# Kernel optimization log

Measured on AMD Instinct MI355X. Metric: run time of the kernel, lower is better.

## Reference

```python
import jax, jax.numpy as jnp
import numpy as np

DIM = 1024
NUM_HEADS = 16
HEAD_DIM = DIM // NUM_HEADS


def setup_inputs() -> dict:
    key = jax.random.key(0)
    k_x, k_q, k_k, k_v, k_o = jax.random.split(key, 5)
    B, L = 2, 2048
    scale = 1.0 / np.sqrt(DIM)
    x_bld = jax.random.normal(k_x, (B, L, DIM), dtype=jnp.float32)
    # LinearGeneral kernels: (in_features, num_heads, head_dim) for q/k/v,
    # (num_heads, head_dim, out_features) for out. Init ~ lecun_normal-ish scale.
    Wq = jax.random.normal(k_q, (DIM, NUM_HEADS, HEAD_DIM), dtype=jnp.float32) * scale
    Wk = jax.random.normal(k_k, (DIM, NUM_HEADS, HEAD_DIM), dtype=jnp.float32) * scale
    Wv = jax.random.normal(k_v, (DIM, NUM_HEADS, HEAD_DIM), dtype=jnp.float32) * scale
    Wo = jax.random.normal(k_o, (NUM_HEADS, HEAD_DIM, DIM), dtype=jnp.float32) * scale
    return {"x_bld": x_bld, "Wq": Wq, "Wk": Wk, "Wv": Wv, "Wo": Wo}


def reference(x_bld, Wq, Wk, Wv, Wo) -> jnp.ndarray:
    # Projections: [B,L,D] x [D,H,hd] -> [B,L,H,hd]
    q_blhd = jnp.einsum('bld,dhk->blhk', x_bld, Wq)
    k_blhd = jnp.einsum('bld,dhk->blhk', x_bld, Wk)
    v_blhd = jnp.einsum('bld,dhk->blhk', x_bld, Wv)
    # Scores: [B,H,L,L]
    attn_bhll = jnp.einsum('bqhd,bkhd->bhqk', q_blhd, k_blhd)
    attn_bhll = attn_bhll / jnp.sqrt(jnp.asarray(HEAD_DIM, dtype=attn_bhll.dtype))
    L = x_bld.shape[1]
    qi = jnp.arange(L)[:, None]
    ki = jnp.arange(L)[None, :]
    mask_ll = ki <= qi  # causal, no window
    neg_inf = jnp.finfo(attn_bhll.dtype).min
    attn_bhll = jnp.where(mask_ll[None, None, :, :], attn_bhll, neg_inf)
    attn_bhll = jax.nn.softmax(attn_bhll, axis=-1)
    y_blhd = jnp.einsum('bhqk,bkhd->bqhd', attn_bhll, v_blhd)
    # Output projection: contract (H, hd) -> D
    return jnp.einsum('blhk,hkd->bld', y_blhd, Wo)
```

## Files before the change

### kernel.cpp

```cpp
#include <hip/hip_runtime.h>
#include <hip/hip_bf16.h>

typedef __hip_bfloat16 bf16;
typedef __attribute__((ext_vector_type(8))) short short8;
typedef __attribute__((ext_vector_type(4))) float f32x4;
typedef __attribute__((ext_vector_type(4))) unsigned int u32x4;

__device__ __forceinline__ float bfbits2f(unsigned short u) {
    return __uint_as_float(((unsigned int)u) << 16);
}
__device__ __forceinline__ unsigned short f2bfbits(float f) {
    union { float f; unsigned int u; } x;
    x.f = f;
    unsigned int r = x.u + 0x7FFFu + ((x.u >> 16) & 1u);
    return (unsigned short)(r >> 16);
}
__device__ __forceinline__ unsigned int pack_bf16x2(float lo, float hi) {
    unsigned int u0 = __float_as_uint(lo) + 0x8000u;
    unsigned int u1 = __float_as_uint(hi) + 0x8000u;
    return __builtin_amdgcn_perm(u1, u0, 0x07060302u);
}
__device__ __forceinline__ void async_copy16(const void* g, void* l) {
    __builtin_amdgcn_global_load_lds(
        (const __attribute__((address_space(1))) void*)g,
        (__attribute__((address_space(3))) void*)l, 16, 0, 0);
}
__device__ __forceinline__ bool sniff_bf16(const unsigned int* p, int lane) {
    unsigned int wd = p[lane];
    unsigned int e = (wd >> 7) & 0xFFu;
    return __popcll(__ballot(e >= 90u && e <= 150u)) > 40;
}

__global__ __launch_bounds__(256) void prep(
    const void* __restrict__ X, const void* __restrict__ W1,
    const void* __restrict__ W2, const void* __restrict__ W3,
    const void* __restrict__ W4, short* __restrict__ xb,
    short* __restrict__ O1, short* __restrict__ O2,
    short* __restrict__ O3, short* __restrict__ O4) {
    __shared__ float tbuf[32][33];
    const int bx = blockIdx.x;
    const int tid = threadIdx.x;
    const int lane = tid & 63;

    if (bx < 2048) {
        const bool isBf = sniff_bf16((const unsigned int*)X, lane);
        const int i = (bx * 256 + tid) * 8;
        if (isBf) {
            *(short8*)&xb[i] = *(const short8*)((const short*)X + i);
        } else {
            const float* xf = (const float*)X + i;
            float4 a = *(const float4*)xf;
            float4 b = *(const float4*)(xf + 4);
            short8 o;
            o[0] = (short)f2bfbits(a.x); o[1] = (short)f2bfbits(a.y);
            o[2] = (short)f2bfbits(a.z); o[3] = (short)f2bfbits(a.w);
            o[4] = (short)f2bfbits(b.x); o[5] = (short)f2bfbits(b.y);
            o[6] = (short)f2bfbits(b.z); o[7] = (short)f2bfbits(b.w);
            *(short8*)&xb[i] = o;
        }
    } else {
        const void* Ws[4] = {W1, W2, W3, W4};
        short* Os[4] = {O1, O2, O3, O4};
        const int t = bx - 2048;
        const int wsel = t >> 10;
        const int tile = t & 1023;
        const int bxt = tile & 31, byt = tile >> 5;
        const void* W = Ws[wsel];
        const bool isBf = sniff_bf16((const unsigned int*)W, lane);
        const float scale = (wsel == 0) ? 0.18033688f : 1.0f;
        short* O = Os[wsel];

        const int tx = tid & 31, ty = tid >> 5;
        const int gx = bxt * 32 + tx;
#pragma unroll
        for (int i = 0; i < 4; i++) {
            const int gy = byt * 32 + ty + i * 8;
            float v = isBf
                ? bfbits2f(((const unsigned short*)W)[(size_t)gy * 1024 + gx])
                : ((const float*)W)[(size_t)gy * 1024 + gx];
            tbuf[ty + i * 8][tx] = v * scale;
        }
        __syncthreads();
#pragma unroll
        for (int i = 0; i < 4; i++) {
            const int orow = bxt * 32 + ty + i * 8;
            const int ocol = byt * 32 + tx;
            O[(size_t)orow * 1024 + ocol] = (short)f2bfbits(tbuf[tx][ty + i * 8]);
        }
    }
}

__global__ __launch_bounds__(256) void transpose_v(const short* __restrict__ qkv,
                                                   short* __restrict__ VtG) {
    __shared__ short t[32][33];
    const int tx = threadIdx.x & 31, ty = threadIdx.x >> 5;
    const int b = blockIdx.z >> 4, h = blockIdx.z & 15;
    const int l0 = blockIdx.x * 32, d0 = blockIdx.y * 32;
#pragma unroll
    for (int i = 0; i < 4; i++) {
        const int l = l0 + ty + i * 8;
        t[ty + i * 8][tx] =
            qkv[(size_t)(b * 2048 + l) * 3072 + 2048 + h * 64 + d0 + tx];
    }
    __syncthreads();
    const int ptx = 2 * (tx & 15) + (tx >> 4);
#pragma unroll
    for (int i = 0; i < 4; i++) {
        const int d = d0 + ty + i * 8;
        VtG[((size_t)(b * 16 + h) * 64 + d) * 2048 + l0 + ptx] = t[tx][ty + i * 8];
    }
}

template <int BN>
__global__ __launch_bounds__(256) void gemm_async(const short* __restrict__ A,
                                                  const short* __restrict__ Bt,
                                                  void* __restrict__ C,
                                                  const unsigned int* __restrict__ xdet,
                                                  int M, int N, int K) {
    __shared__ short As[2][128 * 32];
    __shared__ short Bs[2][BN * 32];
    constexpr int NI = BN / 32;

    const int tid = threadIdx.x;
    const int lane = tid & 63;
    const int wv = __builtin_amdgcn_readfirstlane(tid >> 6);
    const int quad = lane >> 4, l16 = lane & 15;
    const int wr = wv >> 1, wc = wv & 1;
    const int m0 = blockIdx.y * 128, n0 = blockIdx.x * BN;

    const int gr = lane >> 2;
    const int gc = ((lane & 3) ^ ((lane >> 3) & 3)) * 8;

    const f32x4 zero = {0.f, 0.f, 0.f, 0.f};
    f32x4 acc[4][NI];
#pragma unroll
    for (int mi = 0; mi < 4; mi++)
#pragma unroll
        for (int ni = 0; ni < NI; ni++) acc[mi][ni] = zero;

    const short* aptr[2];
    const short* bptr[BN / 64];
#pragma unroll
    for (int t = 0; t < 2; t++)
        aptr[t] = A + (size_t)(m0 + t * 64 + wv * 16 + gr) * K + gc;
#pragma unroll
    for (int t = 0; t < BN / 64; t++)
        bptr[t] = Bt + (size_t)(n0 + t * 64 + wv * 16 + gr) * K + gc;

#pragma unroll
    for (int t = 0; t < 2; t++) async_copy16(aptr[t], &As[0][(t * 64 + wv * 16) * 32]);
#pragma unroll
    for (int t = 0; t < BN / 64; t++) async_copy16(bptr[t], &Bs[0][(t * 64 + wv * 16) * 32]);

    const int ss = (quad ^ ((l16 >> 1) & 3)) * 8;

    for (int k0 = 0; k0 < K; k0 += 32) {
        const int cur = (k0 >> 5) & 1;
        __syncthreads();
        if (k0 + 32 < K) {
            const int nxt = cur ^ 1;
#pragma unroll
            for (int t = 0; t < 2; t++)
                async_copy16(aptr[t] + k0 + 32, &As[nxt][(t * 64 + wv * 16) * 32]);
#pragma unroll
            for (int t = 0; t < BN / 64; t++)
                async_copy16(bptr[t] + k0 + 32, &Bs[nxt][(t * 64 + wv * 16) * 32]);
        }

        short8 af[4], bfv[NI];
#pragma unroll
        for (int mi = 0; mi < 4; mi++)
            af[mi] = *(const short8*)&As[cur][(wr * 64 + mi * 16 + l16) * 32 + ss];
#pragma unroll
        for (int ni = 0; ni < NI; ni++)
            bfv[ni] = *(const short8*)&Bs[cur][(wc * (BN / 2) + ni * 16 + l16) * 32 + ss];
#pragma unroll
        for (int mi = 0; mi < 4; mi++)
#pragma unroll
            for (int ni = 0; ni < NI; ni++)
                acc[mi][ni] = __builtin_amdgcn_mfma_f32_16x16x32_bf16(
                    af[mi], bfv[ni], acc[mi][ni], 0, 0, 0);
    }

    bool outBf = true;
    if (xdet) outBf = sniff_bf16(xdet, lane);
    if (outBf) {
        unsigned short* Cb = (unsigned short*)C;
#pragma unroll
        for (int mi = 0; mi < 4; mi++)
#pragma unroll
            for (int ni = 0; ni < NI; ni++)
#pragma unroll
                for (int r = 0; r < 4; r++) {
                    const int row = m0 + wr * 64 + mi * 16 + quad * 4 + r;
                    const int col = n0 + wc * (BN / 2) + ni * 16 + l16;
                    Cb[(size_t)row * N + col] = f2bfbits(acc[mi][ni][r]);
                }
    } else {
        float* Cf = (float*)C;
#pragma unroll
        for (int mi = 0; mi < 4; mi++)
#pragma unroll
            for (int ni = 0; ni < NI; ni++)
#pragma unroll
                for (int r = 0; r < 4; r++) {
                    const int row = m0 + wr * 64 + mi * 16 + quad * 4 + r;
                    const int col = n0 + wc * (BN / 2) + ni * 16 + l16;
                    Cf[(size_t)row * N + col] = acc[mi][ni][r];
                }
    }
}

__global__ __launch_bounds__(128) void attn_mfma8(
    const short* __restrict__ qkv, const short* __restrict__ VtG,
    short* __restrict__ Yg, short* __restrict__ Opart, float* __restrict__ ml) {
    __shared__ float scr[4][16][68];
    __shared__ float lred[2][64];

    const int tid = threadIdx.x;
    const int lane = tid & 63;
    const int wv = __builtin_amdgcn_readfirstlane(tid >> 6);
    const int quad = lane >> 4, l16 = lane & 15;
    const int bh = blockIdx.x;
    const int b = bh >> 4, h = bh & 15;

    int qb, seg, S;
    const int slot = blockIdx.y;
    if (slot < 64)      { qb = 31 - (slot >> 2); seg = slot & 3; S = 4; }
    else if (slot < 80) { const int t2 = slot - 64; qb = 15 - (t2 >> 1); seg = t2 & 1; S = 2; }
    else                { qb = 87 - slot; seg = 0; S = 1; }

    const int ns = qb + 1;
    const int sb0 = seg * ns / S;
    const int sb1 = (seg + 1) * ns / S;
    const int w32 = wv * 32;

    short8 qf[4][2];
    {
        const short* qbase = qkv + (size_t)(b * 2048 + qb * 64 + l16) * 3072 +
                             h * 64 + quad * 8;
#pragma unroll
        for (int qt = 0; qt < 4; qt++)
#pragma unroll
            for (int hf = 0; hf < 2; hf++)
                qf[qt][hf] = *(const short8*)(qbase + qt * 16 * 3072 + hf * 32);
    }

    const size_t KSTEP = (size_t)64 * 3072;
    const short* kb[2];
#pragma unroll
    for (int kt = 0; kt < 2; kt++)
        kb[kt] = qkv + (size_t)(b * 2048 + sb0 * 64 + w32 + kt * 16 + l16) * 3072 +
                 1024 + h * 64 + quad * 8;
    const short* vb[4];
#pragma unroll
    for (int dt = 0; dt < 4; dt++)
        vb[dt] = VtG + ((size_t)bh * 64 + dt * 16 + l16) * 2048 + sb0 * 64 + w32 +
                 quad * 8;

    f32x4 O[4][4];
#pragma unroll
    for (int qt = 0; qt < 4; qt++)
#pragma unroll
        for (int dt = 0; dt < 4; dt++) O[qt][dt] = {0.f, 0.f, 0.f, 0.f};
    float lp[4] = {0.f, 0.f, 0.f, 0.f};

    const f32x4 minit = {-17.3123405f, -17.3123405f, -17.3123405f, -17.3123405f};
    const int keyoff0 = w32 + quad * 4;

    auto LOADK = [&](short8 (&kf)[2][2], short8 (&vf)[4]) {
#pragma unroll
        for (int kt = 0; kt < 2; kt++) {
#pragma unroll
            for (int hf = 0; hf < 2; hf++)
                kf[kt][hf] = *(const short8*)(kb[kt] + hf * 32);
            kb[kt] += KSTEP;
        }
#pragma unroll
        for (int dt = 0; dt < 4; dt++) {
            vf[dt] = *(const short8*)vb[dt];
            vb[dt] += 64;
        }
    };

    auto COMPUTE = [&](const short8 (&kf)[2][2], const short8 (&vf)[4], int sb) {
#pragma unroll
        for (int qt = 0; qt < 4; qt++) {
            f32x4 sA = __builtin_amdgcn_mfma_f32_16x16x32_bf16(kf[0][0], qf[qt][0], minit, 0, 0, 0);
            sA = __builtin_amdgcn_mfma_f32_16x16x32_bf16(kf[0][1], qf[qt][1], sA, 0, 0, 0);
            f32x4 sB = __builtin_amdgcn_mfma_f32_16x16x32_bf16(kf[1][0], qf[qt][0], minit, 0, 0, 0);
            sB = __builtin_amdgcn_mfma_f32_16x16x32_bf16(kf[1][1], qf[qt][1], sB, 0, 0, 0);
            if (sb == qb) {
                const int qcol = qt * 16 + l16;
#pragma unroll
                for (int r = 0; r < 4; r++) {
                    if (keyoff0 + r > qcol) sA[r] = -1e30f;
                    if (keyoff0 + 16 + r > qcol) sB[r] = -1e30f;
                }
            }
            union { u32x4 u; short8 s; } pa;
#pragma unroll
            for (int t = 0; t < 4; t++) {
                sA[t] = __builtin_amdgcn_exp2f(sA[t]);
                sB[t] = __builtin_amdgcn_exp2f(sB[t]);
                lp[qt] += sA[t] + sB[t];
                pa.u[t] = pack_bf16x2(sA[t], sB[t]);
            }
#pragma unroll
            for (int dt = 0; dt < 4; dt++)
                O[qt][dt] = __builtin_amdgcn_mfma_f32_16x16x32_bf16(
                    pa.s, vf[dt], O[qt][dt], 0, 0, 0);
        }
    };

    short8 kA[2][2], vA[4], kB[2][2], vB[4];
    LOADK(kA, vA);
    int sb = sb0;
    while (true) {
        if (sb + 1 < sb1) LOADK(kB, vB);
        COMPUTE(kA, vA, sb);
        if (++sb >= sb1) break;
        if (sb + 1 < sb1) LOADK(kA, vA);
        COMPUTE(kB, vB, sb);
        if (++sb >= sb1) break;
    }

#pragma unroll
    for (int qt = 0; qt < 4; qt++) {
        float v = lp[qt];
        v += __shfl_xor(v, 16);
        v += __shfl_xor(v, 32);
        if (quad == 0) lred[wv][qt * 16 + l16] = v;
    }

#pragma unroll
    for (int qt = 0; qt < 4; qt++) {
        if ((qt >> 1) != wv) {
#pragma unroll
            for (int dt = 0; dt < 4; dt++)
#pragma unroll
                for (int r = 0; r < 4; r++)
                    scr[qt][quad * 4 + r][dt * 16 + l16] = O[qt][dt][r];
        }
    }
    __syncthreads();
#pragma unroll
    for (int qt = 0; qt < 4; qt++) {
        if ((qt >> 1) == wv) {
#pragma unroll
            for (int dt = 0; dt < 4; dt++)
#pragma unroll
                for (int r = 0; r < 4; r++)
                    O[qt][dt][r] += scr[qt][quad * 4 + r][dt * 16 + l16];
        }
    }

    if (S == 1) {
#pragma unroll
        for (int qt = 0; qt < 4; qt++) {
            if ((qt >> 1) == wv) {
#pragma unroll
                for (int r = 0; r < 4; r++) {
                    const int q = qt * 16 + quad * 4 + r;
                    const float inv = 1.f / (lred[0][q] + lred[1][q]);
#pragma unroll
                    for (int dt = 0; dt < 4; dt++)
                        Yg[(size_t)(b * 2048 + qb * 64 + q) * 1024 + h * 64 +
                           dt * 16 + l16] = (short)f2bfbits(O[qt][dt][r] * inv);
                }
            }
        }
    } else {
        const int qidx = qb - 8;
        const int base = ((seg * 32 + bh) * 24 + qidx) * 64;
#pragma unroll
        for (int qt = 0; qt < 4; qt++) {
            if ((qt >> 1) == wv) {
#pragma unroll
                for (int r = 0; r < 4; r++) {
                    const int q = qt * 16 + quad * 4 + r;
#pragma unroll
                    for (int dt = 0; dt < 4; dt++)
                        Opart[(size_t)(base + q) * 64 + dt * 16 + l16] =
                            (short)f2bfbits(O[qt][dt][r]);
                    if (l16 == 0) ml[base + q] = lred[0][q] + lred[1][q];
                }
            }
        }
    }
}

__global__ __launch_bounds__(256) void attn_combine6(
    const short* __restrict__ Opart, const float* __restrict__ ml,
    short* __restrict__ Yg) {
    const int qb = 8 + blockIdx.x;
    const int bh = blockIdx.y;
    const int b = bh >> 4, h = bh & 15;
    const int S = (qb >= 16) ? 4 : 2;
    const int qidx = qb - 8;
    const int tid = threadIdx.x;
    const int q = tid >> 2;
    const int d0 = (tid & 3) * 16;

    float a0[8] = {}, a1[8] = {};
    float lsum = 0.f;
    for (int s = 0; s < S; s++) {
        const int idx = ((s * 32 + bh) * 24 + qidx) * 64 + q;
        lsum += ml[idx];
        const short* p = Opart + (size_t)idx * 64 + d0;
        short8 x0 = *(const short8*)p;
        short8 x1 = *(const short8*)(p + 8);
#pragma unroll
        for (int t = 0; t < 8; t++) {
            a0[t] += bfbits2f((unsigned short)x0[t]);
            a1[t] += bfbits2f((unsigned short)x1[t]);
        }
    }
    const float inv = 1.f / lsum;
    short8 o0, o1;
#pragma unroll
    for (int t = 0; t < 8; t++) {
        o0[t] = (short)f2bfbits(a0[t] * inv);
        o1[t] = (short)f2bfbits(a1[t] * inv);
    }
    short* yp = Yg + (size_t)(b * 2048 + qb * 64 + q) * 1024 + h * 64 + d0;
    *(short8*)yp = o0;
    *(short8*)(yp + 8) = o1;
}

extern "C" void kernel_launch(void* const* d_in, const int* in_sizes, int n_in,
                              void* d_out, int out_size, void* d_ws, size_t ws_size,
                              hipStream_t stream) {
    const int M = 2 * 2048;
    const int D = 1024;

    char* w = (char*)d_ws;
    short* xb  = (short*)w;
    short* WqT = (short*)(w + (8u << 20));
    short* WkT = WqT + (1u << 20);
    short* WvT = WkT + (1u << 20);
    short* WoT = WvT + (1u << 20);
    short* qkv = WoT + (1u << 20);
    short* VtG = qkv + (size_t)M * 3072;
    short* Opart = VtG + (size_t)2048 * 2048;
    float* mlp = (float*)(Opart + (size_t)4 * 32 * 24 * 64 * 64);
    short* y = xb;

    prep<<<6144, 256, 0, stream>>>(d_in[0], d_in[1], d_in[2], d_in[3], d_in[4],
                                   xb, WqT, WkT, WvT, WoT);

    gemm_async<128><<<dim3(3072 / 128, M / 128), 256, 0, stream>>>(
        xb, WqT, qkv, nullptr, M, 3072, D);

    transpose_v<<<dim3(64, 2, 32), 256, 0, stream>>>(qkv, VtG);

    attn_mfma8<<<dim3(32, 88), 128, 0, stream>>>(qkv, VtG, y, Opart, mlp);
    attn_combine6<<<dim3(24, 32), 256, 0, stream>>>(Opart, mlp, y);

    gemm_async<64><<<dim3(D / 64, M / 128), 256, 0, stream>>>(
        y, WoT, d_out, (const unsigned int*)d_in[0], M, D, D);
}
```

Before: 209.7 us.

## Stage K/V tiles in double-buffered LDS and split attention across four waves

The attention kernel now runs 256 threads as a 2x2 wave grid: two waves split the query rows and two split the keys of each block. K and V^T tiles are loaded once per block into a swizzled, double-buffered LDS with async global-to-LDS copies instead of each wave loading fragments straight from global memory. The aim is to share K/V loads across waves and raise parallelism per block. The cost is a barrier every key block and a serialized cross-wave reduction of O through LDS that takes several barriers.

```diff
diff --git a/kernel.cpp b/kernel.cpp
--- a/kernel.cpp
+++ b/kernel.cpp
@@ -211,15 +211,18 @@
     }
 }
 
-__global__ __launch_bounds__(128) void attn_mfma8(
+__global__ __launch_bounds__(256) void attn_mfma9(
     const short* __restrict__ qkv, const short* __restrict__ VtG,
     short* __restrict__ Yg, short* __restrict__ Opart, float* __restrict__ ml) {
-    __shared__ float scr[4][16][68];
+    __shared__ short Ks[2][64 * 64];
+    __shared__ short Vt[2][64 * 64];
+    __shared__ float scr[16][68];
     __shared__ float lred[2][64];
 
     const int tid = threadIdx.x;
     const int lane = tid & 63;
     const int wv = __builtin_amdgcn_readfirstlane(tid >> 6);
+    const int wvq = wv >> 1, wvk = wv & 1;
     const int quad = lane >> 4, l16 = lane & 15;
     const int bh = blockIdx.x;
     const int b = bh >> 4, h = bh & 15;
@@ -233,69 +236,96 @@
     const int ns = qb + 1;
     const int sb0 = seg * ns / S;
     const int sb1 = (seg + 1) * ns / S;
-    const int w32 = wv * 32;
-
-    short8 qf[4][2];
+
+    const int rr = lane >> 3;
+    const int scol = ((lane & 7) ^ rr) * 8;
+
+    const short* kptr[2];
+    const short* vptr[2];
+    short* kdst[2];
+    short* vdst[2];
+#pragma unroll
+    for (int i = 0; i < 2; i++) {
+        const int u = wv * 2 + i;
+        kptr[i] = qkv + (size_t)(b * 2048 + sb0 * 64 + u * 8 + rr) * 3072 + 1024 +
+                  h * 64 + scol;
+        kdst[i] = &Ks[0][(u * 8) * 64];
+        vptr[i] = VtG + ((size_t)bh * 64 + u * 8 + rr) * 2048 + sb0 * 64 + scol;
+        vdst[i] = &Vt[0][(u * 8) * 64];
+    }
+    const int bufoff = 64 * 64;
+    const int buf0 = sb0 & 1;
+
+#pragma unroll
+    for (int i = 0; i < 2; i++) {
+        async_copy16(kptr[i], kdst[i] + buf0 * bufoff);
+        async_copy16(vptr[i], vdst[i] + buf0 * bufoff);
+        kptr[i] += 64 * 3072;
+        vptr[i] += 64;
+    }
+    short8 qf[2][2];
     {
-        const short* qbase = qkv + (size_t)(b * 2048 + qb * 64 + l16) * 3072 +
+        const short* qbase = qkv + (size_t)(b * 2048 + qb * 64 + wvq * 32 + l16) * 3072 +
                              h * 64 + quad * 8;
 #pragma unroll
-        for (int qt = 0; qt < 4; qt++)
+        for (int qt = 0; qt < 2; qt++)
 #pragma unroll
             for (int hf = 0; hf < 2; hf++)
                 qf[qt][hf] = *(const short8*)(qbase + qt * 16 * 3072 + hf * 32);
     }
-
-    const size_t KSTEP = (size_t)64 * 3072;
-    const short* kb[2];
-#pragma unroll
-    for (int kt = 0; kt < 2; kt++)
-        kb[kt] = qkv + (size_t)(b * 2048 + sb0 * 64 + w32 + kt * 16 + l16) * 3072 +
-                 1024 + h * 64 + quad * 8;
-    const short* vb[4];
-#pragma unroll
-    for (int dt = 0; dt < 4; dt++)
-        vb[dt] = VtG + ((size_t)bh * 64 + dt * 16 + l16) * 2048 + sb0 * 64 + w32 +
-                 quad * 8;
-
-    f32x4 O[4][4];
-#pragma unroll
-    for (int qt = 0; qt < 4; qt++)
+    __syncthreads();
+
+    const int sl = (quad ^ (l16 & 7)) * 8;
+
+    const f32x4 minit = {-17.3123405f, -17.3123405f, -17.3123405f, -17.3123405f};
+    f32x4 O[2][4];
+#pragma unroll
+    for (int qt = 0; qt < 2; qt++)
 #pragma unroll
         for (int dt = 0; dt < 4; dt++) O[qt][dt] = {0.f, 0.f, 0.f, 0.f};
-    float lp[4] = {0.f, 0.f, 0.f, 0.f};
-
-    const f32x4 minit = {-17.3123405f, -17.3123405f, -17.3123405f, -17.3123405f};
-    const int keyoff0 = w32 + quad * 4;
-
-    auto LOADK = [&](short8 (&kf)[2][2], short8 (&vf)[4]) {
-#pragma unroll
-        for (int kt = 0; kt < 2; kt++) {
+    float lp[2] = {0.f, 0.f};
+    const int keyA0 = wvk * 32 + quad * 4;
+
+    for (int sb = sb0; sb < sb1; sb++) {
+        const int cur = sb & 1;
+        if (sb != sb0) __syncthreads();
+        if (sb + 1 < sb1) {
+            const int nxt = cur ^ 1;
+#pragma unroll
+            for (int i = 0; i < 2; i++) {
+                async_copy16(kptr[i], kdst[i] + nxt * bufoff);
+                async_copy16(vptr[i], vdst[i] + nxt * bufoff);
+                kptr[i] += 64 * 3072;
+                vptr[i] += 64;
+            }
+        }
+        const short* Kc = &Ks[cur][0];
+        const short* Vc = &Vt[cur][0];
+
+        short8 kf[2][2], vf[4];
+#pragma unroll
+        for (int kt = 0; kt < 2; kt++)
 #pragma unroll
             for (int hf = 0; hf < 2; hf++)
-                kf[kt][hf] = *(const short8*)(kb[kt] + hf * 32);
-            kb[kt] += KSTEP;
-        }
-#pragma unroll
-        for (int dt = 0; dt < 4; dt++) {
-            vf[dt] = *(const short8*)vb[dt];
-            vb[dt] += 64;
-        }
-    };
-
-    auto COMPUTE = [&](const short8 (&kf)[2][2], const short8 (&vf)[4], int sb) {
-#pragma unroll
-        for (int qt = 0; qt < 4; qt++) {
+                kf[kt][hf] = *(const short8*)
+                    &Kc[(wvk * 32 + kt * 16 + l16) * 64 + (sl ^ (hf << 5))];
+#pragma unroll
+        for (int dt = 0; dt < 4; dt++)
+            vf[dt] = *(const short8*)
+                &Vc[(dt * 16 + l16) * 64 + (sl ^ (wvk << 5))];
+
+#pragma unroll
+        for (int qt = 0; qt < 2; qt++) {
             f32x4 sA = __builtin_amdgcn_mfma_f32_16x16x32_bf16(kf[0][0], qf[qt][0], minit, 0, 0, 0);
             sA = __builtin_amdgcn_mfma_f32_16x16x32_bf16(kf[0][1], qf[qt][1], sA, 0, 0, 0);
             f32x4 sB = __builtin_amdgcn_mfma_f32_16x16x32_bf16(kf[1][0], qf[qt][0], minit, 0, 0, 0);
             sB = __builtin_amdgcn_mfma_f32_16x16x32_bf16(kf[1][1], qf[qt][1], sB, 0, 0, 0);
             if (sb == qb) {
-                const int qcol = qt * 16 + l16;
+                const int qcol = wvq * 32 + qt * 16 + l16;
 #pragma unroll
                 for (int r = 0; r < 4; r++) {
-                    if (keyoff0 + r > qcol) sA[r] = -1e30f;
-                    if (keyoff0 + 16 + r > qcol) sB[r] = -1e30f;
+                    if (keyA0 + r > qcol) sA[r] = -1e30f;
+                    if (keyA0 + 16 + r > qcol) sB[r] = -1e30f;
                 }
             }
             union { u32x4 u; short8 s; } pa;
@@ -311,81 +341,65 @@
                 O[qt][dt] = __builtin_amdgcn_mfma_f32_16x16x32_bf16(
                     pa.s, vf[dt], O[qt][dt], 0, 0, 0);
         }
-    };
-
-    short8 kA[2][2], vA[4], kB[2][2], vB[4];
-    LOADK(kA, vA);
-    int sb = sb0;
-    while (true) {
-        if (sb + 1 < sb1) LOADK(kB, vB);
-        COMPUTE(kA, vA, sb);
-        if (++sb >= sb1) break;
-        if (sb + 1 < sb1) LOADK(kA, vA);
-        COMPUTE(kB, vB, sb);
-        if (++sb >= sb1) break;
-    }
-
-#pragma unroll
-    for (int qt = 0; qt < 4; qt++) {
+    }
+
+#pragma unroll
+    for (int qt = 0; qt < 2; qt++) {
         float v = lp[qt];
         v += __shfl_xor(v, 16);
         v += __shfl_xor(v, 32);
-        if (quad == 0) lred[wv][qt * 16 + l16] = v;
-    }
-
-#pragma unroll
-    for (int qt = 0; qt < 4; qt++) {
-        if ((qt >> 1) != wv) {
-#pragma unroll
-            for (int dt = 0; dt < 4; dt++)
-#pragma unroll
-                for (int r = 0; r < 4; r++)
-                    scr[qt][quad * 4 + r][dt * 16 + l16] = O[qt][dt][r];
-        }
-    }
-    __syncthreads();
-#pragma unroll
-    for (int qt = 0; qt < 4; qt++) {
-        if ((qt >> 1) == wv) {
-#pragma unroll
-            for (int dt = 0; dt < 4; dt++)
-#pragma unroll
-                for (int r = 0; r < 4; r++)
-                    O[qt][dt][r] += scr[qt][quad * 4 + r][dt * 16 + l16];
-        }
-    }
-
-    if (S == 1) {
-#pragma unroll
-        for (int qt = 0; qt < 4; qt++) {
-            if ((qt >> 1) == wv) {
+        if (quad == 0) lred[wvk][wvq * 32 + qt * 16 + l16] = v;
+    }
+
+#pragma unroll
+    for (int g = 0; g < 2; g++)
+#pragma unroll
+        for (int qt = 0; qt < 2; qt++) {
+            __syncthreads();
+            if (wvq == g && wvk == 1) {
+#pragma unroll
+                for (int dt = 0; dt < 4; dt++)
+#pragma unroll
+                    for (int r = 0; r < 4; r++)
+                        scr[quad * 4 + r][dt * 16 + l16] = O[qt][dt][r];
+            }
+            __syncthreads();
+            if (wvq == g && wvk == 0) {
+#pragma unroll
+                for (int dt = 0; dt < 4; dt++)
+#pragma unroll
+                    for (int r = 0; r < 4; r++)
+                        O[qt][dt][r] += scr[quad * 4 + r][dt * 16 + l16];
+            }
+        }
+
+    if (wvk == 0) {
+        if (S == 1) {
+#pragma unroll
+            for (int qt = 0; qt < 2; qt++)
 #pragma unroll
                 for (int r = 0; r < 4; r++) {
-                    const int q = qt * 16 + quad * 4 + r;
+                    const int q = wvq * 32 + qt * 16 + quad * 4 + r;
                     const float inv = 1.f / (lred[0][q] + lred[1][q]);
 #pragma unroll
                     for (int dt = 0; dt < 4; dt++)
                         Yg[(size_t)(b * 2048 + qb * 64 + q) * 1024 + h * 64 +
                            dt * 16 + l16] = (short)f2bfbits(O[qt][dt][r] * inv);
                 }
-            }
-        }
-    } else {
-        const int qidx = qb - 8;
-        const int base = ((seg * 32 + bh) * 24 + qidx) * 64;
-#pragma unroll
-        for (int qt = 0; qt < 4; qt++) {
-            if ((qt >> 1) == wv) {
+        } else {
+            const int qidx = qb - 8;
+            const int base = ((seg * 32 + bh) * 24 + qidx) * 64;
+#pragma unroll
+            for (int qt = 0; qt < 2; qt++)
 #pragma unroll
                 for (int r = 0; r < 4; r++) {
-                    const int q = qt * 16 + quad * 4 + r;
+                    const int q = wvq * 32 + qt * 16 + quad * 4 + r;
 #pragma unroll
                     for (int dt = 0; dt < 4; dt++)
                         Opart[(size_t)(base + q) * 64 + dt * 16 + l16] =
                             (short)f2bfbits(O[qt][dt][r]);
                     if (l16 == 0) ml[base + q] = lred[0][q] + lred[1][q];
                 }
-            }
         }
     }
 }
@@ -454,7 +468,7 @@
 
     transpose_v<<<dim3(64, 2, 32), 256, 0, stream>>>(qkv, VtG);
 
-    attn_mfma8<<<dim3(32, 88), 128, 0, stream>>>(qkv, VtG, y, Opart, mlp);
+    attn_mfma9<<<dim3(32, 88), 256, 0, stream>>>(qkv, VtG, y, Opart, mlp);
     attn_combine6<<<dim3(24, 32), 256, 0, stream>>>(Opart, mlp, y);
 
     gemm_async<64><<<dim3(D / 64, M / 128), 256, 0, stream>>>(
```

Result: faster. 189.9 us (-9.5%).
